# Performance work log

Measured on AMD Instinct MI355X. Metric: run time of the kernel, lower is better.

## Reference

```python
import jax, jax.numpy as jnp
import numpy as np


def setup_inputs() -> dict:
    key = jax.random.key(0)
    ks = jax.random.split(key, 7)
    B, T, E, D = 4, 4096, 1024, 64
    s = 1.0 / np.sqrt(E)
    return {
        "x": jax.random.normal(ks[0], (B, T, E), dtype=jnp.float32),
        "Wq": jax.random.normal(ks[1], (E, D), dtype=jnp.float32) * s,
        "bq": jnp.zeros((D,), dtype=jnp.float32),
        "Wk": jax.random.normal(ks[2], (E, D), dtype=jnp.float32) * s,
        "bk": jnp.zeros((D,), dtype=jnp.float32),
        "Wv": jax.random.normal(ks[3], (E, D), dtype=jnp.float32) * s,
        "bv": jnp.zeros((D,), dtype=jnp.float32),
    }


def reference(x, Wq, bq, Wk, bk, Wv, bv):
    # Linear projections (torch Linear with W stored as [in, out])
    q = x @ Wq + bq  # [B, T, D]
    k = x @ Wk + bk  # [B, T, D]
    v = x @ Wv + bv  # [B, T, D]
    d_k = q.shape[-1]
    scale = 1.0 / jnp.sqrt(jnp.asarray(d_k, dtype=q.dtype))
    scores = jnp.einsum("btd,bsd->bts", q, k) * scale  # [B, T, T]
    att = jax.nn.softmax(scores, axis=-1)
    # dropout p=0.0 -> identity (eval-mode reference)
    out = jnp.einsum("bts,bsd->btd", att, v)  # [B, T, D]
    return out
```

## Files before the change

kernel.cpp:

```cpp
#include <hip/hip_runtime.h>

typedef __attribute__((ext_vector_type(4))) float f32x4;
typedef __attribute__((ext_vector_type(16))) float f32x16;
typedef __attribute__((ext_vector_type(8))) short s16x8;
typedef __attribute__((ext_vector_type(4))) short s16x4;
typedef __attribute__((ext_vector_type(4))) unsigned u32x4;

#define BATCH 4
#define SEQ 4096
#define EMB 1024
#define HD 64
#define QSCALE (0.125f * 1.44269504088896f)

static __device__ __forceinline__ unsigned short f2bf(float f) {
  union { float f; unsigned int u; } a;
  a.f = f;
  unsigned int u = a.u;
  u += 0x7FFFu + ((u >> 16) & 1u);
  return (unsigned short)(u >> 16);
}

static __device__ __forceinline__ float fexp2(float x) {
  float r;
  asm("v_exp_f32 %0, %1\n\ts_nop 0" : "=v"(r) : "v"(x));
  return r;
}
static __device__ __forceinline__ void swap32f(float& a, float& b) {
  asm("s_nop 0\n\tv_permlane32_swap_b32 %0, %1\n\ts_nop 0" : "+v"(a), "+v"(b));
}
static __device__ __forceinline__ void swap32u(unsigned& a, unsigned& b) {
  asm("s_nop 0\n\tv_permlane32_swap_b32 %0, %1\n\ts_nop 0" : "+v"(a), "+v"(b));
}
static __device__ __forceinline__ unsigned cvtpk(float lo, float hi) {
  unsigned r;
  asm("v_cvt_pk_bf16_f32 %0, %1, %2" : "=v"(r) : "v"(lo), "v"(hi));
  return r;
}

#define GLL16(g, l)                                                        \
  __builtin_amdgcn_global_load_lds(                                        \
      (const __attribute__((address_space(1))) unsigned int*)(g),          \
      (__attribute__((address_space(3))) unsigned int*)(l), 16, 0, 0)

__global__ __launch_bounds__(256) void k_wt(const float* __restrict__ Wq,
                                            const float* __restrict__ Wk,
                                            const float* __restrict__ Wv,
                                            unsigned short* __restrict__ wt) {
  __shared__ float lds[64][65];
  int tid = threadIdx.x;
  int which = blockIdx.x >> 4;
  int kt = blockIdx.x & 15;
  const float* W = (which == 0) ? Wq : ((which == 1) ? Wk : Wv);
#pragma unroll
  for (int i = 0; i < 4; ++i) {
    int idx = i * 256 + tid;
    int row = idx >> 4, c4 = idx & 15;
    float4 v = *(const float4*)(W + (size_t)(kt * 64 + row) * 64 + c4 * 4);
    lds[row][c4 * 4 + 0] = v.x;
    lds[row][c4 * 4 + 1] = v.y;
    lds[row][c4 * 4 + 2] = v.z;
    lds[row][c4 * 4 + 3] = v.w;
  }
  __syncthreads();
#pragma unroll
  for (int i = 0; i < 2; ++i) {
    int c = i * 256 + tid;
    int cfl = c >> 7, kk = (c >> 6) & 1, l = c & 63;
    int lg = l >> 4, lc = l & 15;
    s16x8 v;
#pragma unroll
    for (int j = 0; j < 8; ++j) v[j] = (short)f2bf(lds[kk * 32 + lg * 8 + j][cfl * 16 + lc]);
    size_t off = ((((size_t)kt * 12 + (which * 4 + cfl)) * 2 + kk) * 64 + l) * 8;
    *(s16x8*)(wt + off) = v;
  }
}

__global__ __launch_bounds__(256, 2) void k_proj(const float* __restrict__ x,
                                                 const unsigned short* __restrict__ wt,
                                                 const float* __restrict__ bq,
                                                 const float* __restrict__ bk,
                                                 const float* __restrict__ bv,
                                                 unsigned short* __restrict__ qws,
                                                 unsigned short* __restrict__ kws,
                                                 unsigned short* __restrict__ vws) {
  __shared__ char xb[4][8192];
  int tid = threadIdx.x;
  int w = tid >> 6, ln = tid & 63;
  int lg = ln >> 4, lc = ln & 15;
  int m0 = blockIdx.x * 32;

  f32x4 acc[2][3];
#pragma unroll
  for (int s = 0; s < 2; ++s)
#pragma unroll
    for (int c = 0; c < 3; ++c) acc[s][c] = (f32x4){0.f, 0.f, 0.f, 0.f};

  s16x8 bA[3][2], bB[3][2];

  int srow = w * 8 + (ln >> 4);
  int schunk0 = ln & 15;
#define GLLI(kt_, bi_)                                                        \
  _Pragma("unroll") for (int p = 0; p < 2; ++p) {                             \
    int r = srow + p * 4;                                                     \
    const char* src = (const char*)x + (size_t)(m0 + r) * 4096 + (kt_)*256 +  \
                      ((schunk0 ^ (r & 7)) << 4);                             \
    GLL16(src, &xb[bi_][w * 2048 + p * 1024]);                                \
  }
#define BLD(dst_, kt_)                                                        \
  _Pragma("unroll") for (int c = 0; c < 3; ++c)                               \
      _Pragma("unroll") for (int kk = 0; kk < 2; ++kk)                        \
          dst_[c][kk] = *(const s16x8*)(wt + ((size_t)((kt_)*12 + w * 3 + c) * 2 + kk) * 512 + ln * 8);

#define ITER(T_, bcur_, bnext_, NW_)                                          \
  {                                                                           \
    if ((T_) + 1 < 16) BLD(bnext_, (T_) + 1);                                 \
    if ((T_) + 3 < 16) GLLI((T_) + 3, ((T_) + 3) & 3);                        \
    asm volatile("s_waitcnt vmcnt(" #NW_ ")" ::: "memory");                   \
    __builtin_amdgcn_s_barrier();                                             \
    __builtin_amdgcn_sched_barrier(0);                                        \
    s16x8 a[2][2];                                                            \
    _Pragma("unroll") for (int s = 0; s < 2; ++s)                             \
        _Pragma("unroll") for (int kk = 0; kk < 2; ++kk) {                    \
      int g0 = kk * 8 + lg * 2;                                               \
      f32x4 c0 = *(const f32x4*)(&xb[(T_) & 3][(s * 16 + lc) * 256 + ((g0 ^ (lc & 7)) << 4)]); \
      f32x4 c1 = *(const f32x4*)(&xb[(T_) & 3][(s * 16 + lc) * 256 + (((g0 + 1) ^ (lc & 7)) << 4)]); \
      union { u32x4 u; s16x8 v; } cv;                                         \
      cv.u = (u32x4){cvtpk(c0[0], c0[1]), cvtpk(c0[2], c0[3]),                \
                     cvtpk(c1[0], c1[1]), cvtpk(c1[2], c1[3])};               \
      a[s][kk] = cv.v;                                                        \
    }                                                                         \
    __builtin_amdgcn_s_setprio(1);                                            \
    _Pragma("unroll") for (int s = 0; s < 2; ++s)                             \
        _Pragma("unroll") for (int c = 0; c < 3; ++c)                         \
            _Pragma("unroll") for (int kk = 0; kk < 2; ++kk)                  \
                acc[s][c] = __builtin_amdgcn_mfma_f32_16x16x32_bf16(          \
                    a[s][kk], bcur_[c][kk], acc[s][c], 0, 0, 0);              \
    __builtin_amdgcn_s_setprio(0);                                            \
    __builtin_amdgcn_s_barrier();                                             \
  }

  GLLI(0, 0);
  GLLI(1, 1);
  GLLI(2, 2);
  BLD(bA, 0);
  ITER(0, bA, bB, 18)
  ITER(1, bB, bA, 24)
  ITER(2, bA, bB, 30)
  ITER(3, bB, bA, 24)
  ITER(4, bA, bB, 24)
  ITER(5, bB, bA, 24)
  ITER(6, bA, bB, 24)
  ITER(7, bB, bA, 24)
  ITER(8, bA, bB, 24)
  ITER(9, bB, bA, 24)
  ITER(10, bA, bB, 24)
  ITER(11, bB, bA, 24)
  ITER(12, bA, bB, 24)
  ITER(13, bB, bA, 22)
  ITER(14, bA, bB, 20)
  ITER(15, bB, bA, 12)
#undef GLLI
#undef BLD
#undef ITER

  unsigned short* ep = (unsigned short*)&xb[0][0];
#pragma unroll
  for (int c = 0; c < 3; ++c) {
    int cf = w * 3 + c;
    int which = cf >> 2;
    int ncol = (cf & 3) * 16 + lc;
    float bias = (which == 0) ? bq[ncol] : ((which == 1) ? bk[ncol] : bv[ncol]);
    if (which < 2) {
#pragma unroll
      for (int s = 0; s < 2; ++s)
#pragma unroll
        for (int r = 0; r < 4; ++r) {
          int trow = s * 16 + lg * 4 + r;
          float val = acc[s][c][r] + bias;
          if (which == 0) val *= QSCALE;
          int o = (ncol >> 4) * 512 + ((ncol >> 3) & 1) * 256 + trow * 8 + (ncol & 7);
          ep[which * 2048 + o] = f2bf(val);
        }
    } else {
#pragma unroll
      for (int s = 0; s < 2; ++s) {
        s16x4 pk;
#pragma unroll
        for (int r = 0; r < 4; ++r) pk[r] = (short)f2bf(acc[s][c][r] + bias);
        int o = s * 1024 + (ncol >> 5) * 512 + (lg >> 1) * 256 + (ncol & 31) * 8 + (lg & 1) * 4;
        *(s16x4*)(ep + 2 * 2048 + o) = pk;
      }
    }
  }
  __syncthreads();
  {
    int b = m0 >> 12, tt = m0 & 4095;
    unsigned short* qdst = qws + (size_t)b * SEQ * 64 + (tt >> 5) * 2048;
    unsigned short* kdst = kws + (size_t)b * SEQ * 64 + (tt >> 5) * 2048;
    unsigned short* vdst = vws + (size_t)b * SEQ * 64 + (tt >> 4) * 1024;
#pragma unroll
    for (int k = 0; k < 3; ++k) {
      int u = k * 256 + tid;
      s16x8 val = *(const s16x8*)(ep + u * 8);
      int which = u >> 8;
      int o = (u & 255) * 8;
      unsigned short* dst = (which == 0) ? qdst : ((which == 1) ? kdst : vdst);
      *(s16x8*)(dst + o) = val;
    }
  }
}

template <int NS>
__global__ __launch_bounds__(256, 2) void k_attn(const unsigned short* __restrict__ qf_g,
                                                 const unsigned short* __restrict__ kf_g,
                                                 const unsigned short* __restrict__ vf_g,
                                                 float* __restrict__ part,
                                                 float2* __restrict__ ml) {
  __shared__ char kv[2][16384];
  int tid = threadIdx.x;
  int w = tid >> 6, ln = tid & 63;
  int F = blockIdx.x;
  int chunk = 8 * NS;
  int idx = (F & 7) * chunk + (F >> 3);
  int split = idx >> 6;
  int rem = idx & 63;
  int b = rem >> 4, q16 = rem & 15;
  const int TPS = 64 / NS;
  int t0 = split * TPS;
  int tlast = t0 + TPS - 1;

  const unsigned short* qb = qf_g + (size_t)b * SEQ * 64;
  const char* kbytes = (const char*)(kf_g + (size_t)b * SEQ * 64);
  const char* vbytes = (const char*)(vf_g + (size_t)b * SEQ * 64);

  int qrow = q16 * 256 + w * 64;

  s16x8 qf[2][4];
#pragma unroll
  for (int sub = 0; sub < 2; ++sub)
#pragma unroll
    for (int db = 0; db < 4; ++db)
      qf[sub][db] = *(const s16x8*)(qb + (size_t)(((q16 * 8 + w * 2 + sub) * 4 + db) * 512 + ln * 8));

  f32x16 o_[2][2];
#pragma unroll
  for (int sub = 0; sub < 2; ++sub)
#pragma unroll
    for (int dt = 0; dt < 2; ++dt)
#pragma unroll
      for (int i = 0; i < 16; ++i) o_[sub][dt][i] = 0.f;
  float m_[2] = {-1e30f, -1e30f}, l_[2] = {0.f, 0.f};

#define STAGE(t_, bi_)                                                        \
  _Pragma("unroll") for (int i = 0; i < 4; ++i) {                             \
    int cc = w * 4 + i;                                                       \
    const char* src = (cc < 8 ? kbytes + (size_t)(t_)*8192 + cc * 1024        \
                              : vbytes + (size_t)(t_)*8192 + (cc - 8) * 1024) \
                      + ln * 16;                                              \
    GLL16(src, &kv[bi_][cc * 1024]);                                          \
  }

  STAGE(t0, 0)
#pragma unroll 1
  for (int t = t0; t <= tlast; ++t) {
    int bi = (t - t0) & 1;
    if (t < tlast) {
      STAGE(t + 1, bi ^ 1)
      asm volatile("s_waitcnt vmcnt(4)" ::: "memory");
    } else {
      asm volatile("s_waitcnt vmcnt(0)" ::: "memory");
    }
    __builtin_amdgcn_s_barrier();
    __builtin_amdgcn_sched_barrier(0);

    s16x8 kfc[2][4];
#pragma unroll
    for (int kt = 0; kt < 2; ++kt)
#pragma unroll
      for (int db = 0; db < 4; ++db)
        kfc[kt][db] = *(const s16x8*)(&kv[bi][(kt * 4 + db) * 1024 + ln * 16]);

    f32x16 s0[2];
    __builtin_amdgcn_s_setprio(1);
#pragma unroll
    for (int kt = 0; kt < 2; ++kt) {
      f32x16 a = {0.f, 0.f, 0.f, 0.f, 0.f, 0.f, 0.f, 0.f,
                  0.f, 0.f, 0.f, 0.f, 0.f, 0.f, 0.f, 0.f};
#pragma unroll
      for (int db = 0; db < 4; ++db)
        a = __builtin_amdgcn_mfma_f32_32x32x16_bf16(kfc[kt][db], qf[0][db], a, 0, 0, 0);
      s0[kt] = a;
    }
    __builtin_amdgcn_s_setprio(0);

    s16x8 vf[4][2];
#pragma unroll
    for (int k4 = 0; k4 < 4; ++k4)
#pragma unroll
      for (int dt = 0; dt < 2; ++dt)
        vf[k4][dt] = *(const s16x8*)(&kv[bi][8192 + (k4 * 2 + dt) * 1024 + ln * 16]);

    s16x8 pf[2][4];
#define SOFTMAX_PACK(S_, SUBIDX)                                               \
    {                                                                          \
      float mx[16];                                                            \
      _Pragma("unroll") for (int i = 0; i < 16; ++i)                           \
          mx[i] = fmaxf(S_[0][i], S_[1][i]);                                   \
      _Pragma("unroll") for (int i = 0; i < 8; ++i) mx[i] = fmaxf(mx[i], mx[i + 8]); \
      _Pragma("unroll") for (int i = 0; i < 4; ++i) mx[i] = fmaxf(mx[i], mx[i + 4]); \
      float tm = fmaxf(fmaxf(mx[0], mx[1]), fmaxf(mx[2], mx[3]));              \
      float ta = tm, tb = tm;                                                  \
      swap32f(ta, tb);                                                         \
      tm = fmaxf(ta, tb);                                                      \
      if (!__all(tm <= m_[SUBIDX] + 8.0f)) {                                   \
        float mn = fmaxf(m_[SUBIDX], tm);                                      \
        float al = fexp2(m_[SUBIDX] - mn);                                     \
        _Pragma("unroll") for (int dt = 0; dt < 2; ++dt)                       \
            _Pragma("unroll") for (int i = 0; i < 16; ++i) o_[SUBIDX][dt][i] *= al; \
        l_[SUBIDX] *= al;                                                      \
        m_[SUBIDX] = mn;                                                       \
      }                                                                        \
      float mm = m_[SUBIDX];                                                   \
      _Pragma("unroll") for (int kt = 0; kt < 2; ++kt)                         \
          _Pragma("unroll") for (int i = 0; i < 16; ++i)                       \
              S_[kt][i] = fexp2(S_[kt][i] - mm);                               \
      float sm[16];                                                            \
      _Pragma("unroll") for (int i = 0; i < 16; ++i) sm[i] = S_[0][i] + S_[1][i]; \
      _Pragma("unroll") for (int i = 0; i < 8; ++i) sm[i] += sm[i + 8];        \
      _Pragma("unroll") for (int i = 0; i < 4; ++i) sm[i] += sm[i + 4];        \
      float ts = (sm[0] + sm[1]) + (sm[2] + sm[3]);                            \
      float sa = ts, sb = ts;                                                  \
      swap32f(sa, sb);                                                         \
      l_[SUBIDX] += sa + sb;                                                   \
      _Pragma("unroll") for (int k4 = 0; k4 < 4; ++k4) {                       \
        int kt = k4 >> 1, mr = 2 * (k4 & 1);                                   \
        unsigned a0 = cvtpk(S_[kt][mr * 4 + 0], S_[kt][mr * 4 + 1]);           \
        unsigned a1 = cvtpk(S_[kt][mr * 4 + 2], S_[kt][mr * 4 + 3]);           \
        unsigned b0 = cvtpk(S_[kt][mr * 4 + 4], S_[kt][mr * 4 + 5]);           \
        unsigned b1 = cvtpk(S_[kt][mr * 4 + 6], S_[kt][mr * 4 + 7]);           \
        swap32u(a0, b0);                                                       \
        swap32u(a1, b1);                                                       \
        union { u32x4 u; s16x8 v16; } cvt;                                     \
        cvt.u = (u32x4){a0, a1, b0, b1};                                       \
        pf[SUBIDX][k4] = cvt.v16;                                              \
      }                                                                        \
    }

    SOFTMAX_PACK(s0, 0)

    f32x16 s1[2];
    __builtin_amdgcn_s_setprio(1);
#pragma unroll
    for (int kt = 0; kt < 2; ++kt) {
      f32x16 a = {0.f, 0.f, 0.f, 0.f, 0.f, 0.f, 0.f, 0.f,
                  0.f, 0.f, 0.f, 0.f, 0.f, 0.f, 0.f, 0.f};
#pragma unroll
      for (int db = 0; db < 4; ++db)
        a = __builtin_amdgcn_mfma_f32_32x32x16_bf16(kfc[kt][db], qf[1][db], a, 0, 0, 0);
      s1[kt] = a;
    }
    __builtin_amdgcn_s_setprio(0);

    SOFTMAX_PACK(s1, 1)
#undef SOFTMAX_PACK

    __builtin_amdgcn_s_setprio(1);
#pragma unroll
    for (int sub = 0; sub < 2; ++sub)
#pragma unroll
      for (int dt = 0; dt < 2; ++dt)
#pragma unroll
        for (int k4 = 0; k4 < 4; ++k4)
          o_[sub][dt] = __builtin_amdgcn_mfma_f32_32x32x16_bf16(vf[k4][dt], pf[sub][k4],
                                                                o_[sub][dt], 0, 0, 0);
    __builtin_amdgcn_s_setprio(0);
    __builtin_amdgcn_s_barrier();
  }
#undef STAGE

  float* pb = part + (size_t)(split * 4 + b) * 64 * SEQ;
  int hi = ln >> 5, lq = ln & 31;
#pragma unroll
  for (int sub = 0; sub < 2; ++sub) {
    int tq = qrow + sub * 32 + lq;
#pragma unroll
    for (int dt = 0; dt < 2; ++dt)
#pragma unroll
      for (int re = 0; re < 16; ++re) {
        int d = dt * 32 + (re & 3) + 8 * (re >> 2) + 4 * hi;
        pb[(size_t)d * SEQ + tq] = o_[sub][dt][re];
      }
  }
  if (ln < 32) {
#pragma unroll
    for (int sub = 0; sub < 2; ++sub)
      ml[(size_t)(split * 4 + b) * SEQ + qrow + sub * 32 + ln] = make_float2(m_[sub], l_[sub]);
  }
}

template <int NS>
__global__ __launch_bounds__(256) void k_red(const float* __restrict__ part,
                                             const float2* __restrict__ ml,
                                             float* __restrict__ out) {
  __shared__ float lds[64][65];
  int tid = threadIdx.x;
  int w = tid >> 6, ln = tid & 63;
  int t0 = blockIdx.x * 64;
  int b = t0 >> 12, tt = t0 & 4095;
  int t = tt + ln;

  float2 mls[NS];
#pragma unroll
  for (int s = 0; s < NS; ++s) mls[s] = ml[(size_t)(s * 4 + b) * SEQ + t];
  float M = mls[0].x;
#pragma unroll
  for (int s = 1; s < NS; ++s) M = fmaxf(M, mls[s].x);
  float Lden = 0.f;
#pragma unroll
  for (int s = 0; s < NS; ++s) Lden += mls[s].y * fexp2(mls[s].x - M);
  float inv = 1.0f / Lden;
  float sc[NS];
#pragma unroll
  for (int s = 0; s < NS; ++s) sc[s] = fexp2(mls[s].x - M) * inv;

  float acc[16];
#pragma unroll
  for (int i = 0; i < 16; ++i) acc[i] = 0.f;
#pragma unroll
  for (int s = 0; s < NS; ++s) {
    const float* pb = part + ((size_t)(s * 4 + b) * 64 + w * 16) * SEQ + t;
#pragma unroll
    for (int i = 0; i < 16; ++i) acc[i] += sc[s] * pb[(size_t)i * SEQ];
  }
#pragma unroll
  for (int i = 0; i < 16; ++i) lds[w * 16 + i][ln] = acc[i];
  __syncthreads();
#pragma unroll
  for (int r = 0; r < 16; ++r)
    out[(size_t)(t0 + w * 16 + r) * 64 + ln] = lds[ln][w * 16 + r];
}

extern "C" void kernel_launch(void* const* d_in, const int* in_sizes, int n_in,
                              void* d_out, int out_size, void* d_ws, size_t ws_size,
                              hipStream_t stream) {
  const float* x = (const float*)d_in[0];
  const float* Wq = (const float*)d_in[1];
  const float* bq = (const float*)d_in[2];
  const float* Wk = (const float*)d_in[3];
  const float* bk = (const float*)d_in[4];
  const float* Wv = (const float*)d_in[5];
  const float* bv = (const float*)d_in[6];
  float* out = (float*)d_out;

  char* ws = (char*)d_ws;
  unsigned short* wt = (unsigned short*)(ws);
  unsigned short* qws = (unsigned short*)(ws + 0x80000);
  unsigned short* kws = (unsigned short*)(ws + 0x280000);
  unsigned short* vws = (unsigned short*)(ws + 0x480000);
  const size_t base = 0x680000;
  const size_t perSplit = (size_t)16384 * 64 * 4 + (size_t)16384 * 8;

  k_wt<<<48, 256, 0, stream>>>(Wq, Wk, Wv, wt);
  k_proj<<<512, 256, 0, stream>>>(x, wt, bq, bk, bv, qws, kws, vws);

#define RUN_NS(NSV)                                                           \
  {                                                                           \
    float* partp = (float*)(ws + base);                                       \
    float2* mlp = (float2*)(ws + base + (size_t)NSV * 16384 * 64 * 4);        \
    k_attn<NSV><<<64 * NSV, 256, 0, stream>>>(qws, kws, vws, partp, mlp);     \
    k_red<NSV><<<256, 256, 0, stream>>>(partp, mlp, out);                     \
  }

  if (ws_size >= base + 8 * perSplit) {
    RUN_NS(8)
  } else if (ws_size >= base + 4 * perSplit) {
    RUN_NS(4)
  } else if (ws_size >= base + 2 * perSplit) {
    RUN_NS(2)
  } else {
    RUN_NS(1)
  }
#undef RUN_NS
}
```

Before: 62.08 us.

## Halve per-wave query rows in attention, double grid, split reduction finer

The attention kernel now gives each wave 32 query rows instead of 64, which doubles the number of blocks and raises the occupancy hint from 2 to 3 blocks per CU. V fragments are read from LDS inside the PV MFMA loop instead of being preloaded, which lowers register pressure. The reduction kernel splits each 64-token tile across 4 blocks over head-dim quarters and writes the output with vector stores. exp2 now uses the builtin instead of inline asm. The trade-off is that each K/V tile loaded into LDS is reused by half as many query rows, so K/V global traffic and staging work double relative to compute.

```diff
diff --git a/kernel.cpp b/kernel.cpp
--- a/kernel.cpp
+++ b/kernel.cpp
@@ -21,9 +21,7 @@
 }
 
 static __device__ __forceinline__ float fexp2(float x) {
-  float r;
-  asm("v_exp_f32 %0, %1\n\ts_nop 0" : "=v"(r) : "v"(x));
-  return r;
+  return __builtin_amdgcn_exp2f(x);
 }
 static __device__ __forceinline__ void swap32f(float& a, float& b) {
   asm("s_nop 0\n\tv_permlane32_swap_b32 %0, %1\n\ts_nop 0" : "+v"(a), "+v"(b));
@@ -211,7 +209,7 @@
 }
 
 template <int NS>
-__global__ __launch_bounds__(256, 2) void k_attn(const unsigned short* __restrict__ qf_g,
+__global__ __launch_bounds__(256, 3) void k_attn(const unsigned short* __restrict__ qf_g,
                                                  const unsigned short* __restrict__ kf_g,
                                                  const unsigned short* __restrict__ vf_g,
                                                  float* __restrict__ part,
@@ -220,11 +218,11 @@
   int tid = threadIdx.x;
   int w = tid >> 6, ln = tid & 63;
   int F = blockIdx.x;
-  int chunk = 8 * NS;
-  int idx = (F & 7) * chunk + (F >> 3);
-  int split = idx >> 6;
-  int rem = idx & 63;
-  int b = rem >> 4, q16 = rem & 15;
+  const int nb = 128 * NS;
+  int idx = (F & 7) * (nb >> 3) + (F >> 3);
+  int split = idx >> 7;
+  int rem = idx & 127;
+  int b = rem >> 5, q7 = rem & 31;
   const int TPS = 64 / NS;
   int t0 = split * TPS;
   int tlast = t0 + TPS - 1;
@@ -233,23 +231,19 @@
   const char* kbytes = (const char*)(kf_g + (size_t)b * SEQ * 64);
   const char* vbytes = (const char*)(vf_g + (size_t)b * SEQ * 64);
 
-  int qrow = q16 * 256 + w * 64;
-
-  s16x8 qf[2][4];
-#pragma unroll
-  for (int sub = 0; sub < 2; ++sub)
-#pragma unroll
-    for (int db = 0; db < 4; ++db)
-      qf[sub][db] = *(const s16x8*)(qb + (size_t)(((q16 * 8 + w * 2 + sub) * 4 + db) * 512 + ln * 8));
-
-  f32x16 o_[2][2];
-#pragma unroll
-  for (int sub = 0; sub < 2; ++sub)
-#pragma unroll
-    for (int dt = 0; dt < 2; ++dt)
-#pragma unroll
-      for (int i = 0; i < 16; ++i) o_[sub][dt][i] = 0.f;
-  float m_[2] = {-1e30f, -1e30f}, l_[2] = {0.f, 0.f};
+  int qrow = q7 * 128 + w * 32;
+
+  s16x8 qf[4];
+#pragma unroll
+  for (int db = 0; db < 4; ++db)
+    qf[db] = *(const s16x8*)(qb + (size_t)(((q7 * 4 + w) * 4 + db) * 512 + ln * 8));
+
+  f32x16 o_[2];
+#pragma unroll
+  for (int dt = 0; dt < 2; ++dt)
+#pragma unroll
+    for (int i = 0; i < 16; ++i) o_[dt][i] = 0.f;
+  float m_ = -1e30f, l_ = 0.f;
 
 #define STAGE(t_, bi_)                                                        \
   _Pragma("unroll") for (int i = 0; i < 4; ++i) {                             \
@@ -280,7 +274,7 @@
       for (int db = 0; db < 4; ++db)
         kfc[kt][db] = *(const s16x8*)(&kv[bi][(kt * 4 + db) * 1024 + ln * 16]);
 
-    f32x16 s0[2];
+    f32x16 s[2];
     __builtin_amdgcn_s_setprio(1);
 #pragma unroll
     for (int kt = 0; kt < 2; ++kt) {
@@ -288,91 +282,73 @@
                   0.f, 0.f, 0.f, 0.f, 0.f, 0.f, 0.f, 0.f};
 #pragma unroll
       for (int db = 0; db < 4; ++db)
-        a = __builtin_amdgcn_mfma_f32_32x32x16_bf16(kfc[kt][db], qf[0][db], a, 0, 0, 0);
-      s0[kt] = a;
+        a = __builtin_amdgcn_mfma_f32_32x32x16_bf16(kfc[kt][db], qf[db], a, 0, 0, 0);
+      s[kt] = a;
     }
     __builtin_amdgcn_s_setprio(0);
 
-    s16x8 vf[4][2];
-#pragma unroll
-    for (int k4 = 0; k4 < 4; ++k4)
-#pragma unroll
-      for (int dt = 0; dt < 2; ++dt)
-        vf[k4][dt] = *(const s16x8*)(&kv[bi][8192 + (k4 * 2 + dt) * 1024 + ln * 16]);
-
-    s16x8 pf[2][4];
-#define SOFTMAX_PACK(S_, SUBIDX)                                               \
-    {                                                                          \
-      float mx[16];                                                            \
-      _Pragma("unroll") for (int i = 0; i < 16; ++i)                           \
-          mx[i] = fmaxf(S_[0][i], S_[1][i]);                                   \
-      _Pragma("unroll") for (int i = 0; i < 8; ++i) mx[i] = fmaxf(mx[i], mx[i + 8]); \
-      _Pragma("unroll") for (int i = 0; i < 4; ++i) mx[i] = fmaxf(mx[i], mx[i + 4]); \
-      float tm = fmaxf(fmaxf(mx[0], mx[1]), fmaxf(mx[2], mx[3]));              \
-      float ta = tm, tb = tm;                                                  \
-      swap32f(ta, tb);                                                         \
-      tm = fmaxf(ta, tb);                                                      \
-      if (!__all(tm <= m_[SUBIDX] + 8.0f)) {                                   \
-        float mn = fmaxf(m_[SUBIDX], tm);                                      \
-        float al = fexp2(m_[SUBIDX] - mn);                                     \
-        _Pragma("unroll") for (int dt = 0; dt < 2; ++dt)                       \
-            _Pragma("unroll") for (int i = 0; i < 16; ++i) o_[SUBIDX][dt][i] *= al; \
-        l_[SUBIDX] *= al;                                                      \
-        m_[SUBIDX] = mn;                                                       \
-      }                                                                        \
-      float mm = m_[SUBIDX];                                                   \
-      _Pragma("unroll") for (int kt = 0; kt < 2; ++kt)                         \
-          _Pragma("unroll") for (int i = 0; i < 16; ++i)                       \
-              S_[kt][i] = fexp2(S_[kt][i] - mm);                               \
-      float sm[16];                                                            \
-      _Pragma("unroll") for (int i = 0; i < 16; ++i) sm[i] = S_[0][i] + S_[1][i]; \
-      _Pragma("unroll") for (int i = 0; i < 8; ++i) sm[i] += sm[i + 8];        \
-      _Pragma("unroll") for (int i = 0; i < 4; ++i) sm[i] += sm[i + 4];        \
-      float ts = (sm[0] + sm[1]) + (sm[2] + sm[3]);                            \
-      float sa = ts, sb = ts;                                                  \
-      swap32f(sa, sb);                                                         \
-      l_[SUBIDX] += sa + sb;                                                   \
-      _Pragma("unroll") for (int k4 = 0; k4 < 4; ++k4) {                       \
-        int kt = k4 >> 1, mr = 2 * (k4 & 1);                                   \
-        unsigned a0 = cvtpk(S_[kt][mr * 4 + 0], S_[kt][mr * 4 + 1]);           \
-        unsigned a1 = cvtpk(S_[kt][mr * 4 + 2], S_[kt][mr * 4 + 3]);           \
-        unsigned b0 = cvtpk(S_[kt][mr * 4 + 4], S_[kt][mr * 4 + 5]);           \
-        unsigned b1 = cvtpk(S_[kt][mr * 4 + 6], S_[kt][mr * 4 + 7]);           \
-        swap32u(a0, b0);                                                       \
-        swap32u(a1, b1);                                                       \
-        union { u32x4 u; s16x8 v16; } cvt;                                     \
-        cvt.u = (u32x4){a0, a1, b0, b1};                                       \
-        pf[SUBIDX][k4] = cvt.v16;                                              \
-      }                                                                        \
-    }
-
-    SOFTMAX_PACK(s0, 0)
-
-    f32x16 s1[2];
+    s16x8 pf[4];
+    {
+      float mx[16];
+#pragma unroll
+      for (int i = 0; i < 16; ++i) mx[i] = fmaxf(s[0][i], s[1][i]);
+#pragma unroll
+      for (int i = 0; i < 8; ++i) mx[i] = fmaxf(mx[i], mx[i + 8]);
+#pragma unroll
+      for (int i = 0; i < 4; ++i) mx[i] = fmaxf(mx[i], mx[i + 4]);
+      float tm = fmaxf(fmaxf(mx[0], mx[1]), fmaxf(mx[2], mx[3]));
+      float ta = tm, tb = tm;
+      swap32f(ta, tb);
+      tm = fmaxf(ta, tb);
+      if (!__all(tm <= m_ + 8.0f)) {
+        float mn = fmaxf(m_, tm);
+        float al = fexp2(m_ - mn);
+#pragma unroll
+        for (int dt = 0; dt < 2; ++dt)
+#pragma unroll
+          for (int i = 0; i < 16; ++i) o_[dt][i] *= al;
+        l_ *= al;
+        m_ = mn;
+      }
+      float mm = m_;
+#pragma unroll
+      for (int kt = 0; kt < 2; ++kt)
+#pragma unroll
+        for (int i = 0; i < 16; ++i) s[kt][i] = fexp2(s[kt][i] - mm);
+      float sm[16];
+#pragma unroll
+      for (int i = 0; i < 16; ++i) sm[i] = s[0][i] + s[1][i];
+#pragma unroll
+      for (int i = 0; i < 8; ++i) sm[i] += sm[i + 8];
+#pragma unroll
+      for (int i = 0; i < 4; ++i) sm[i] += sm[i + 4];
+      float ts = (sm[0] + sm[1]) + (sm[2] + sm[3]);
+      float sa = ts, sb = ts;
+      swap32f(sa, sb);
+      l_ += sa + sb;
+#pragma unroll
+      for (int k4 = 0; k4 < 4; ++k4) {
+        int kt = k4 >> 1, mr = 2 * (k4 & 1);
+        unsigned a0 = cvtpk(s[kt][mr * 4 + 0], s[kt][mr * 4 + 1]);
+        unsigned a1 = cvtpk(s[kt][mr * 4 + 2], s[kt][mr * 4 + 3]);
+        unsigned b0 = cvtpk(s[kt][mr * 4 + 4], s[kt][mr * 4 + 5]);
+        unsigned b1 = cvtpk(s[kt][mr * 4 + 6], s[kt][mr * 4 + 7]);
+        swap32u(a0, b0);
+        swap32u(a1, b1);
+        union { u32x4 u; s16x8 v16; } cvt;
+        cvt.u = (u32x4){a0, a1, b0, b1};
+        pf[k4] = cvt.v16;
+      }
+    }
+
     __builtin_amdgcn_s_setprio(1);
 #pragma unroll
-    for (int kt = 0; kt < 2; ++kt) {
-      f32x16 a = {0.f, 0.f, 0.f, 0.f, 0.f, 0.f, 0.f, 0.f,
-                  0.f, 0.f, 0.f, 0.f, 0.f, 0.f, 0.f, 0.f};
-#pragma unroll
-      for (int db = 0; db < 4; ++db)
-        a = __builtin_amdgcn_mfma_f32_32x32x16_bf16(kfc[kt][db], qf[1][db], a, 0, 0, 0);
-      s1[kt] = a;
-    }
-    __builtin_amdgcn_s_setprio(0);
-
-    SOFTMAX_PACK(s1, 1)
-#undef SOFTMAX_PACK
-
-    __builtin_amdgcn_s_setprio(1);
-#pragma unroll
-    for (int sub = 0; sub < 2; ++sub)
-#pragma unroll
-      for (int dt = 0; dt < 2; ++dt)
-#pragma unroll
-        for (int k4 = 0; k4 < 4; ++k4)
-          o_[sub][dt] = __builtin_amdgcn_mfma_f32_32x32x16_bf16(vf[k4][dt], pf[sub][k4],
-                                                                o_[sub][dt], 0, 0, 0);
+    for (int dt = 0; dt < 2; ++dt)
+#pragma unroll
+      for (int k4 = 0; k4 < 4; ++k4) {
+        s16x8 vfr = *(const s16x8*)(&kv[bi][8192 + (k4 * 2 + dt) * 1024 + ln * 16]);
+        o_[dt] = __builtin_amdgcn_mfma_f32_32x32x16_bf16(vfr, pf[k4], o_[dt], 0, 0, 0);
+      }
     __builtin_amdgcn_s_setprio(0);
     __builtin_amdgcn_s_barrier();
   }
@@ -380,38 +356,33 @@
 
   float* pb = part + (size_t)(split * 4 + b) * 64 * SEQ;
   int hi = ln >> 5, lq = ln & 31;
-#pragma unroll
-  for (int sub = 0; sub < 2; ++sub) {
-    int tq = qrow + sub * 32 + lq;
-#pragma unroll
-    for (int dt = 0; dt < 2; ++dt)
-#pragma unroll
-      for (int re = 0; re < 16; ++re) {
-        int d = dt * 32 + (re & 3) + 8 * (re >> 2) + 4 * hi;
-        pb[(size_t)d * SEQ + tq] = o_[sub][dt][re];
-      }
-  }
-  if (ln < 32) {
-#pragma unroll
-    for (int sub = 0; sub < 2; ++sub)
-      ml[(size_t)(split * 4 + b) * SEQ + qrow + sub * 32 + ln] = make_float2(m_[sub], l_[sub]);
-  }
+  int tq = qrow + lq;
+#pragma unroll
+  for (int dt = 0; dt < 2; ++dt)
+#pragma unroll
+    for (int re = 0; re < 16; ++re) {
+      int d = dt * 32 + (re & 3) + 8 * (re >> 2) + 4 * hi;
+      pb[(size_t)d * SEQ + tq] = o_[dt][re];
+    }
+  if (ln < 32)
+    ml[(size_t)(split * 4 + b) * SEQ + qrow + ln] = make_float2(m_, l_);
 }
 
 template <int NS>
 __global__ __launch_bounds__(256) void k_red(const float* __restrict__ part,
                                              const float2* __restrict__ ml,
                                              float* __restrict__ out) {
-  __shared__ float lds[64][65];
+  __shared__ float lds[16][65];
   int tid = threadIdx.x;
   int w = tid >> 6, ln = tid & 63;
-  int t0 = blockIdx.x * 64;
-  int b = t0 >> 12, tt = t0 & 4095;
-  int t = tt + ln;
+  int dq = blockIdx.x & 3;
+  int t0 = (blockIdx.x >> 2) * 64;
+  int b = t0 >> 12;
+  int tt = (t0 & 4095) + ln;
 
   float2 mls[NS];
 #pragma unroll
-  for (int s = 0; s < NS; ++s) mls[s] = ml[(size_t)(s * 4 + b) * SEQ + t];
+  for (int s = 0; s < NS; ++s) mls[s] = ml[(size_t)(s * 4 + b) * SEQ + tt];
   float M = mls[0].x;
 #pragma unroll
   for (int s = 1; s < NS; ++s) M = fmaxf(M, mls[s].x);
@@ -423,21 +394,23 @@
 #pragma unroll
   for (int s = 0; s < NS; ++s) sc[s] = fexp2(mls[s].x - M) * inv;
 
-  float acc[16];
-#pragma unroll
-  for (int i = 0; i < 16; ++i) acc[i] = 0.f;
+  float acc[4] = {0.f, 0.f, 0.f, 0.f};
 #pragma unroll
   for (int s = 0; s < NS; ++s) {
-    const float* pb = part + ((size_t)(s * 4 + b) * 64 + w * 16) * SEQ + t;
-#pragma unroll
-    for (int i = 0; i < 16; ++i) acc[i] += sc[s] * pb[(size_t)i * SEQ];
-  }
-#pragma unroll
-  for (int i = 0; i < 16; ++i) lds[w * 16 + i][ln] = acc[i];
+    const float* pb = part + ((size_t)(s * 4 + b) * 64 + dq * 16 + w * 4) * SEQ + tt;
+#pragma unroll
+    for (int i = 0; i < 4; ++i) acc[i] += sc[s] * pb[(size_t)i * SEQ];
+  }
+#pragma unroll
+  for (int i = 0; i < 4; ++i) lds[w * 4 + i][ln] = acc[i];
   __syncthreads();
-#pragma unroll
-  for (int r = 0; r < 16; ++r)
-    out[(size_t)(t0 + w * 16 + r) * 64 + ln] = lds[ln][w * 16 + r];
+  {
+    int tr = tid >> 2, dc = tid & 3;
+    f32x4 o;
+#pragma unroll
+    for (int j = 0; j < 4; ++j) o[j] = lds[dc * 4 + j][tr];
+    *(f32x4*)(out + (size_t)(t0 + tr) * 64 + dq * 16 + dc * 4) = o;
+  }
 }
 
 extern "C" void kernel_launch(void* const* d_in, const int* in_sizes, int n_in,
@@ -467,8 +440,8 @@
   {                                                                           \
     float* partp = (float*)(ws + base);                                       \
     float2* mlp = (float2*)(ws + base + (size_t)NSV * 16384 * 64 * 4);        \
-    k_attn<NSV><<<64 * NSV, 256, 0, stream>>>(qws, kws, vws, partp, mlp);     \
-    k_red<NSV><<<256, 256, 0, stream>>>(partp, mlp, out);                     \
+    k_attn<NSV><<<128 * NSV, 256, 0, stream>>>(qws, kws, vws, partp, mlp);    \
+    k_red<NSV><<<1024, 256, 0, stream>>>(partp, mlp, out);                    \
   }
 
   if (ws_size >= base + 8 * perSplit) {
```

New measurement: 63.29 us. About the same (+2.0%).
